# Performance work log

Hardware: AMD Instinct MI355X
Metric: run time of the kernel (lower is better)

## Reference

```python
import jax, jax.numpy as jnp
import numpy as np

# Model dims (match init_kwargs)
H = 4096   # hidden_size (reservoir)
I = 64     # input_size
O = 64     # output_size
B = 1      # batch (ESNs use a single long sequence)
S = 4096   # seq_len
LEAKY = 1.0
SPECTRAL_RADIUS = 0.9
SPARSITY = 0.1
INPUT_SCALING = 1.0


def setup_inputs() -> dict:
    rng = np.random.default_rng(0)
    # Frozen random input weights in [-1, 1] * input_scaling
    W_in = ((rng.random((H, I)) * 2.0 - 1.0) * INPUT_SCALING).astype(np.float32)
    # Sparse reservoir matrix, rescaled to target spectral radius.
    W = (rng.random((H, H)) - 0.5) * (rng.random((H, H)) < SPARSITY)
    # Circular-law estimate of the spectral radius of a sparse uniform(-0.5,0.5)
    # matrix: sr ~ sqrt(H * p * var), var = 1/12. Avoids an O(H^3) eig on 4096^2.
    est_sr = float(np.sqrt(H * SPARSITY / 12.0))
    W_res = (W * (SPECTRAL_RADIUS / est_sr)).astype(np.float32)
    # W_out is zeros before fit() in the original; use small random values so the
    # readout path is numerically non-trivial for kernel testing.
    W_out = (rng.standard_normal((O, 1 + I + H)) * 0.05).astype(np.float32)

    key = jax.random.key(0)
    inputs = jax.random.normal(key, (B, S, I), dtype=jnp.float32)
    return {
        "inputs": inputs,
        "W_in": jnp.asarray(W_in),
        "W_res": jnp.asarray(W_res),
        "W_out": jnp.asarray(W_out),
    }


def reference(inputs, W_in, W_res, W_out):
    # inputs: (B, S, I)
    b, s, _ = inputs.shape
    state0 = jnp.zeros((b, H), dtype=inputs.dtype)
    # Precompute the input projection for all timesteps (batched GEMM),
    # leaving only the sequential state @ W_res.T inside the scan.
    proj_in = jnp.einsum('bsi,hi->sbh', inputs, W_in)  # (S, B, H)

    def step(state, pin_t):
        update = jnp.tanh(pin_t + state @ W_res.T)
        new_state = (1.0 - LEAKY) * state + LEAKY * update
        return new_state, new_state

    _, states = jax.lax.scan(step, state0, proj_in)  # (S, B, H)
    states = jnp.transpose(states, (1, 0, 2))        # (B, S, H)

    bias = jnp.ones((b, s, 1), dtype=inputs.dtype)
    extended = jnp.concatenate([bias, inputs, states], axis=-1)  # (B,S,1+I+H)
    outputs = extended @ W_out.T                                  # (B, S, O)
    return outputs[0], states[0]
```

## Files before the change

### kernel.cpp

```cpp
#include <hip/hip_runtime.h>

#define H 4096
#define IN 64
#define OUTD 64
#define SEQ 4096
#define NBLK 256
#define ROWS_PER_BLK 16
#define NTHR 1024
#define SENT 0x7F7F7F7Fu

__device__ __forceinline__ uint4 cpoll1(const unsigned* p) {
    uint4 v;
    asm volatile("global_load_dwordx4 %0, %1, off sc0 sc1\n\t"
                 "s_waitcnt vmcnt(0)"
                 : "=&v"(v) : "v"(p) : "memory");
    return v;
}
__device__ __forceinline__ void coherent_store_f32(float* p, float v) {
    asm volatile("global_store_dword %0, %1, off sc0 sc1"
                 :: "v"(p), "v"(v) : "memory");
}

__device__ __forceinline__ float row16_allreduce(float x) {
    x += __int_as_float(__builtin_amdgcn_update_dpp(0, __float_as_int(x), 0x128, 0xf, 0xf, false));
    x += __int_as_float(__builtin_amdgcn_update_dpp(0, __float_as_int(x), 0x124, 0xf, 0xf, false));
    x += __int_as_float(__builtin_amdgcn_update_dpp(0, __float_as_int(x), 0x122, 0xf, 0xf, false));
    x += __int_as_float(__builtin_amdgcn_update_dpp(0, __float_as_int(x), 0x121, 0xf, 0xf, false));
    return x;
}
__device__ __forceinline__ float quad4_allreduce(float x) {
    x += __int_as_float(__builtin_amdgcn_update_dpp(0, __float_as_int(x), 0xB1, 0xf, 0xf, false));
    x += __int_as_float(__builtin_amdgcn_update_dpp(0, __float_as_int(x), 0x4E, 0xf, 0xf, false));
    return x;
}

__global__ __launch_bounds__(NTHR, 4)
void esn_scan(const float* __restrict__ inputs,
              const float* __restrict__ W_in,
              const float* __restrict__ W_res,
              float* __restrict__ out_states)
{
    __shared__ alignas(16) float4 s_state4[H / 4];
    __shared__ alignas(16) float s_win[ROWS_PER_BLK][65];
    __shared__ alignas(16) float s_part[2][16][20];
    __shared__ alignas(16) float s_u[IN];

    const int tid  = threadIdx.x;
    const int row0 = blockIdx.x * ROWS_PER_BLK;
    const int wave = tid >> 6;
    const int lane = tid & 63;
    const int rg   = lane >> 4;
    const int cgi  = lane & 15;
    const int col0 = wave * 256 + cgi * 16;

    const int sp    = tid >> 2;
    const int sq    = tid & 3;
    const int sslot = 64 * (sp >> 4) + 16 * sq + (sp & 15);
    const int scol  = sp * 16 + sq * 4;

    for (int idx = tid; idx < ROWS_PER_BLK * IN; idx += NTHR)
        s_win[idx >> 6][idx & 63] = W_in[(size_t)row0 * IN + idx];

    float w[4][16];
#pragma unroll
    for (int j = 0; j < 4; ++j) {
        const float* src = W_res + (size_t)(row0 + 4 * rg + j) * H + col0;
#pragma unroll
        for (int q = 0; q < 4; ++q) {
            float4 v = *(const float4*)(src + 4 * q);
            w[j][4 * q + 0] = v.x; w[j][4 * q + 1] = v.y;
            w[j][4 * q + 2] = v.z; w[j][4 * q + 3] = v.w;
        }
    }
    __syncthreads();

    for (int t = 0; t < SEQ; ++t) {
        const int par = t & 1;
        if (tid < 16)
            ((float4*)s_u)[tid] = ((const float4*)(inputs + (size_t)t * IN))[tid];
        if (t == 0) {
            s_state4[sslot] = make_float4(0.f, 0.f, 0.f, 0.f);
        } else {
            const unsigned* p =
                (const unsigned*)(out_states + (size_t)(t - 1) * H + scol);
            uint4 v = cpoll1(p);
            if ((v.x == SENT) | (v.y == SENT) | (v.z == SENT) | (v.w == SENT)) {
                __builtin_amdgcn_s_sleep(8);
                for (;;) {
                    v = cpoll1(p);
                    if ((v.x != SENT) & (v.y != SENT) &
                        (v.z != SENT) & (v.w != SENT))
                        break;
                    __builtin_amdgcn_s_sleep(2);
                }
            }
            float4 f;
            f.x = __uint_as_float(v.x); f.y = __uint_as_float(v.y);
            f.z = __uint_as_float(v.z); f.w = __uint_as_float(v.w);
            s_state4[sslot] = f;
        }

        float a0 = 0.f, a1 = 0.f, a2 = 0.f, a3 = 0.f;
#pragma unroll
        for (int q = 0; q < 4; ++q) {
            float4 sv = s_state4[wave * 64 + q * 16 + cgi];
            a0 = fmaf(w[0][4*q+0], sv.x, a0); a0 = fmaf(w[0][4*q+1], sv.y, a0);
            a0 = fmaf(w[0][4*q+2], sv.z, a0); a0 = fmaf(w[0][4*q+3], sv.w, a0);
            a1 = fmaf(w[1][4*q+0], sv.x, a1); a1 = fmaf(w[1][4*q+1], sv.y, a1);
            a1 = fmaf(w[1][4*q+2], sv.z, a1); a1 = fmaf(w[1][4*q+3], sv.w, a1);
            a2 = fmaf(w[2][4*q+0], sv.x, a2); a2 = fmaf(w[2][4*q+1], sv.y, a2);
            a2 = fmaf(w[2][4*q+2], sv.z, a2); a2 = fmaf(w[2][4*q+3], sv.w, a2);
            a3 = fmaf(w[3][4*q+0], sv.x, a3); a3 = fmaf(w[3][4*q+1], sv.y, a3);
            a3 = fmaf(w[3][4*q+2], sv.z, a3); a3 = fmaf(w[3][4*q+3], sv.w, a3);
        }
        a0 = row16_allreduce(a0);
        a1 = row16_allreduce(a1);
        a2 = row16_allreduce(a2);
        a3 = row16_allreduce(a3);
        if (cgi == 0) {
            float4 pv; pv.x = a0; pv.y = a1; pv.z = a2; pv.w = a3;
            *(float4*)&s_part[par][wave][4 * rg] = pv;
        }
        __syncthreads();

        if (wave == 0) {
            const int row = lane >> 2;
            const int j   = lane & 3;
            float v = s_part[par][4*j+0][row] + s_part[par][4*j+1][row]
                    + s_part[par][4*j+2][row] + s_part[par][4*j+3][row];
#pragma unroll
            for (int e = 0; e < 16; ++e)
                v = fmaf(s_win[row][16*j + e], s_u[16*j + e], v);
            v = quad4_allreduce(v);
            if (j == 0)
                coherent_store_f32(&out_states[(size_t)t * H + row0 + row],
                                   tanhf(v));
        }
    }
}

__device__ __forceinline__ float wave64_allreduce(float x) {
#pragma unroll
    for (int m = 1; m < 64; m <<= 1) x += __shfl_xor(x, m, 64);
    return x;
}

__global__ __launch_bounds__(NTHR)
void esn_out(const float* __restrict__ inputs,
             const float* __restrict__ W_out,
             const float* __restrict__ states,
             float* __restrict__ outputs)
{
    const int wv   = threadIdx.x >> 6;
    const int lane = threadIdx.x & 63;
    const int s    = blockIdx.x * 16 + wv;
    const int K    = 1 + IN + H;

    const float4* st4 = (const float4*)(states + (size_t)s * H);
    float4 sq[16];
#pragma unroll
    for (int k = 0; k < 16; ++k)
        sq[k] = st4[64 * k + lane];
    float4 iq = make_float4(0.f, 0.f, 0.f, 0.f);
    if (lane < 16)
        iq = ((const float4*)(inputs + (size_t)s * IN))[lane];

    for (int o = 0; o < OUTD; ++o) {
        const float* wrow = W_out + (size_t)o * K;
        float acc = 0.f;
#pragma unroll
        for (int k = 0; k < 16; ++k) {
            float4 wq;
            __builtin_memcpy(&wq, wrow + 65 + 4 * (64 * k + lane), 16);
            acc = fmaf(wq.x, sq[k].x, acc);
            acc = fmaf(wq.y, sq[k].y, acc);
            acc = fmaf(wq.z, sq[k].z, acc);
            acc = fmaf(wq.w, sq[k].w, acc);
        }
        if (lane < 16) {
            float4 wi;
            __builtin_memcpy(&wi, wrow + 1 + 4 * lane, 16);
            acc = fmaf(wi.x, iq.x, acc);
            acc = fmaf(wi.y, iq.y, acc);
            acc = fmaf(wi.z, iq.z, acc);
            acc = fmaf(wi.w, iq.w, acc);
            if (lane == 0) acc += wrow[0];
        }
        acc = wave64_allreduce(acc);
        if (lane == 0) outputs[(size_t)s * OUTD + o] = acc;
    }
}

extern "C" void kernel_launch(void* const* d_in, const int* in_sizes, int n_in,
                              void* d_out, int out_size, void* d_ws, size_t ws_size,
                              hipStream_t stream) {
    const float* inputs = (const float*)d_in[0];
    const float* W_in   = (const float*)d_in[1];
    const float* W_res  = (const float*)d_in[2];
    const float* W_out  = (const float*)d_in[3];

    float* outputs = (float*)d_out;
    float* states  = (float*)d_out + (size_t)SEQ * OUTD;

    (void)hipMemsetAsync(states, 0x7F, (size_t)SEQ * H * sizeof(float), stream);

    void* args[] = { (void*)&inputs, (void*)&W_in, (void*)&W_res, (void*)&states };
    (void)hipLaunchCooperativeKernel((void*)esn_scan, dim3(NBLK), dim3(NTHR),
                                     args, 0, stream);

    esn_out<<<dim3(SEQ / 16), dim3(NTHR), 0, stream>>>(inputs, W_out, states, outputs);
}
```

Before: 8.404 ms.

## Fuse readout GEMV into persistent scan kernel using idle waves

```diff
diff --git a/kernel.cpp b/kernel.cpp
--- a/kernel.cpp
+++ b/kernel.cpp
@@ -33,20 +33,29 @@
     x += __int_as_float(__builtin_amdgcn_update_dpp(0, __float_as_int(x), 0x4E, 0xf, 0xf, false));
     return x;
 }
+__device__ __forceinline__ float wave64_allreduce(float x) {
+#pragma unroll
+    for (int m = 1; m < 64; m <<= 1) x += __shfl_xor(x, m, 64);
+    return x;
+}
 
 __global__ __launch_bounds__(NTHR, 4)
 void esn_scan(const float* __restrict__ inputs,
               const float* __restrict__ W_in,
               const float* __restrict__ W_res,
-              float* __restrict__ out_states)
+              const float* __restrict__ W_out,
+              float* __restrict__ out_states,
+              float* __restrict__ outputs)
 {
     __shared__ alignas(16) float4 s_state4[H / 4];
+    __shared__ alignas(16) float4 s_copy[H / 4];
     __shared__ alignas(16) float s_win[ROWS_PER_BLK][65];
     __shared__ alignas(16) float s_part[2][16][20];
     __shared__ alignas(16) float s_u[IN];
 
     const int tid  = threadIdx.x;
-    const int row0 = blockIdx.x * ROWS_PER_BLK;
+    const int bid  = blockIdx.x;
+    const int row0 = bid * ROWS_PER_BLK;
     const int wave = tid >> 6;
     const int lane = tid & 63;
     const int rg   = lane >> 4;
@@ -58,6 +67,35 @@
     const int sslot = 64 * (sp >> 4) + 16 * sq + (sp & 15);
     const int scol  = sp * 16 + sq * 4;
 
+    auto out_dot = [&](int s, int o) {
+        const float* wrow = W_out + (size_t)o * (1 + IN + H);
+        float acc = 0.f;
+#pragma unroll
+        for (int j = 0; j < 16; ++j) {
+            const int qi   = lane + 64 * j;
+            const int slot = 64 * j + 16 * (lane & 3) + ((lane >> 2) & 15);
+            float4 sv = s_copy[slot];
+            float4 wq;
+            __builtin_memcpy(&wq, wrow + 65 + 4 * qi, 16);
+            acc = fmaf(wq.x, sv.x, acc);
+            acc = fmaf(wq.y, sv.y, acc);
+            acc = fmaf(wq.z, sv.z, acc);
+            acc = fmaf(wq.w, sv.w, acc);
+        }
+        if (lane < 16) {
+            float4 wi, iu;
+            __builtin_memcpy(&wi, wrow + 1 + 4 * lane, 16);
+            iu = *(const float4*)(inputs + (size_t)s * IN + 4 * lane);
+            acc = fmaf(wi.x, iu.x, acc);
+            acc = fmaf(wi.y, iu.y, acc);
+            acc = fmaf(wi.z, iu.z, acc);
+            acc = fmaf(wi.w, iu.w, acc);
+            if (lane == 0) acc += wrow[0];
+        }
+        acc = wave64_allreduce(acc);
+        if (lane == 0) outputs[(size_t)s * OUTD + o] = acc;
+    };
+
     for (int idx = tid; idx < ROWS_PER_BLK * IN; idx += NTHR)
         s_win[idx >> 6][idx & 63] = W_in[(size_t)row0 * IN + idx];
 
@@ -78,6 +116,7 @@
         const int par = t & 1;
         if (tid < 16)
             ((float4*)s_u)[tid] = ((const float4*)(inputs + (size_t)t * IN))[tid];
+
         if (t == 0) {
             s_state4[sslot] = make_float4(0.f, 0.f, 0.f, 0.f);
         } else {
@@ -135,59 +174,36 @@
             if (j == 0)
                 coherent_store_f32(&out_states[(size_t)t * H + row0 + row],
                                    tanhf(v));
-        }
+        } else if (wave >= 8 && t >= 1) {
+            const int k = (t - 1 - bid) & 255;
+            if (k >= 1 && k <= 8) {
+                const int s = t - 1 - k;
+                if (s >= 0) out_dot(s, (wave - 8) + 8 * (k - 1));
+            }
+        }
+        if (t >= 1 && (((t - 1 - bid) & 255) == 0))
+            s_copy[tid] = s_state4[tid];
     }
-}
-
-__device__ __forceinline__ float wave64_allreduce(float x) {
-#pragma unroll
-    for (int m = 1; m < 64; m <<= 1) x += __shfl_xor(x, m, 64);
-    return x;
-}
-
-__global__ __launch_bounds__(NTHR)
-void esn_out(const float* __restrict__ inputs,
-             const float* __restrict__ W_out,
-             const float* __restrict__ states,
-             float* __restrict__ outputs)
-{
-    const int wv   = threadIdx.x >> 6;
-    const int lane = threadIdx.x & 63;
-    const int s    = blockIdx.x * 16 + wv;
-    const int K    = 1 + IN + H;
-
-    const float4* st4 = (const float4*)(states + (size_t)s * H);
-    float4 sq[16];
-#pragma unroll
-    for (int k = 0; k < 16; ++k)
-        sq[k] = st4[64 * k + lane];
-    float4 iq = make_float4(0.f, 0.f, 0.f, 0.f);
-    if (lane < 16)
-        iq = ((const float4*)(inputs + (size_t)s * IN))[lane];
-
-    for (int o = 0; o < OUTD; ++o) {
-        const float* wrow = W_out + (size_t)o * K;
-        float acc = 0.f;
-#pragma unroll
-        for (int k = 0; k < 16; ++k) {
-            float4 wq;
-            __builtin_memcpy(&wq, wrow + 65 + 4 * (64 * k + lane), 16);
-            acc = fmaf(wq.x, sq[k].x, acc);
-            acc = fmaf(wq.y, sq[k].y, acc);
-            acc = fmaf(wq.z, sq[k].z, acc);
-            acc = fmaf(wq.w, sq[k].w, acc);
-        }
-        if (lane < 16) {
-            float4 wi;
-            __builtin_memcpy(&wi, wrow + 1 + 4 * lane, 16);
-            acc = fmaf(wi.x, iq.x, acc);
-            acc = fmaf(wi.y, iq.y, acc);
-            acc = fmaf(wi.z, iq.z, acc);
-            acc = fmaf(wi.w, iq.w, acc);
-            if (lane == 0) acc += wrow[0];
-        }
-        acc = wave64_allreduce(acc);
-        if (lane == 0) outputs[(size_t)s * OUTD + o] = acc;
+
+    if (bid >= 247) {
+        const int s = bid + 3840;
+        if (bid == 255) {
+            const unsigned* p =
+                (const unsigned*)(out_states + (size_t)4095 * H + scol);
+            uint4 v = cpoll1(p);
+            while ((v.x == SENT) | (v.y == SENT) | (v.z == SENT) | (v.w == SENT)) {
+                __builtin_amdgcn_s_sleep(2);
+                v = cpoll1(p);
+            }
+            float4 f;
+            f.x = __uint_as_float(v.x); f.y = __uint_as_float(v.y);
+            f.z = __uint_as_float(v.z); f.w = __uint_as_float(v.w);
+            s_copy[sslot] = f;
+        }
+        __syncthreads();
+#pragma unroll
+        for (int i = 0; i < 4; ++i)
+            out_dot(s, wave * 4 + i);
     }
 }
 
@@ -204,9 +220,8 @@
 
     (void)hipMemsetAsync(states, 0x7F, (size_t)SEQ * H * sizeof(float), stream);
 
-    void* args[] = { (void*)&inputs, (void*)&W_in, (void*)&W_res, (void*)&states };
+    void* args[] = { (void*)&inputs, (void*)&W_in, (void*)&W_res,
+                     (void*)&W_out, (void*)&states, (void*)&outputs };
     (void)hipLaunchCooperativeKernel((void*)esn_scan, dim3(NBLK), dim3(NTHR),
                                      args, 0, stream);
-
-    esn_out<<<dim3(SEQ / 16), dim3(NTHR), 0, stream>>>(inputs, W_out, states, outputs);
-}
+}
```

Measured after the change: 14.15 ms. +68.4%, slower.
